# Optimization experiments

Hardware: AMD Instinct MI355X
Metric: run time of the kernel (lower is better)

Reference implementation:

```python
import jax, jax.numpy as jnp
import numpy as np

EPS = 1e-8

def _l2norm(x):
    return x / (jnp.linalg.norm(x, axis=-1, keepdims=True) + EPS)

def setup_inputs() -> dict:
    key = jax.random.key(0)
    k1, k2, k3, k4, k5, k6 = jax.random.split(key, 6)
    NQ, NB, NF = 16384, 128, 64
    HD = 2 * NF
    Q = jax.random.normal(k1, (NQ, HD), dtype=jnp.float32)
    reference_angles = jax.random.uniform(k2, (NF,), dtype=jnp.float32) * 2.0 * np.pi
    probes = jax.random.normal(k3, (NB, HD), dtype=jnp.float32)
    # params: perturb around the torch inits (log(e-1), zeros, zeros) for a non-degenerate test
    init_val = float(np.log(np.e - 1.0))
    q_weights_raw = init_val + 0.1 * jax.random.normal(k4, (NB, NF), dtype=jnp.float32)
    q_magnitude_weights = 0.1 * jax.random.normal(k5, (NB, NF), dtype=jnp.float32)
    q_bias = 0.1 * jax.random.normal(k6, (NB,), dtype=jnp.float32)
    return {"Q": Q, "reference_angles": reference_angles, "probes": probes,
            "q_weights_raw": q_weights_raw, "q_magnitude_weights": q_magnitude_weights,
            "q_bias": q_bias}

def reference(Q, reference_angles, probes, q_weights_raw, q_magnitude_weights, q_bias):
    NF = reference_angles.shape[0]
    # --- shared probe layer: L2 normalize then RoPE-rotate (front/back real/imag layout)
    pn = _l2norm(probes)                      # (B, 2F)
    pr, pi = pn[:, :NF], pn[:, NF:]
    c, s = jnp.cos(reference_angles), jnp.sin(reference_angles)
    P_real = pr * c - pi * s                  # (B, F)
    P_imag = pr * s + pi * c
    # --- distance-based scorer
    Qn = _l2norm(Q)                           # (Nq, 2F)
    Q_real, Q_imag = Qn[:, :NF], Qn[:, NF:]
    err_r = P_real[None, :, :] - Q_real[:, None, :]   # (Nq, B, F)
    err_i = P_imag[None, :, :] - Q_imag[:, None, :]
    distance = jnp.sqrt(err_r ** 2 + err_i ** 2 + EPS)
    eff_w = -jax.nn.softplus(q_weights_raw)           # (B, F), negative weights
    distance_term = jnp.einsum('qbf,bf->qb', distance, eff_w)
    Q_mag = jnp.sqrt(Q_real ** 2 + Q_imag ** 2 + EPS)  # (Nq, F)
    magnitude_term = Q_mag @ q_magnitude_weights.T     # (Nq, B)
    return distance_term + magnitude_term + q_bias
```

## Files before the change

### kernel.cpp

```cpp
#include <hip/hip_runtime.h>

#define NQ 16384
#define NB 128
#define NF 64
#define HD 128
#define EPSF 1e-8f
#define BTILE 8
#define NBT (NB / BTILE)
#define NFP (NF / 2)

typedef float f32x2 __attribute__((ext_vector_type(2)));
typedef float f32x4 __attribute__((ext_vector_type(4)));

struct FP2Row {
    f32x2 x2[BTILE];
    f32x2 y2[BTILE];
    f32x2 z2[BTILE];
    f32x2 w2[BTILE];
    f32x2 m2[BTILE];
};

__global__ __launch_bounds__(256) void prep_kernel(
    const float* __restrict__ Q,
    const float* __restrict__ probes,
    const float* __restrict__ angles,
    const float* __restrict__ qw,
    const float* __restrict__ mw,
    f32x4* __restrict__ qA,
    FP2Row* __restrict__ tab) {
    __shared__ f32x4 sA[8][NFP + 1];
    if (blockIdx.x < 2048) {
        const int qi = threadIdx.x >> 5;
        const int sl = threadIdx.x & 31;
        const int q  = blockIdx.x * 8 + qi;
        const float2* Q2 = (const float2*)Q;
        float2 a = Q2[q * 64 + sl];
        float2 c = Q2[q * 64 + 32 + sl];
        float ss = a.x * a.x + a.y * a.y + c.x * c.x + c.y * c.y;
        #pragma unroll
        for (int m = 1; m < 32; m <<= 1) ss += __shfl_xor(ss, m);
        float inv = 1.0f / (sqrtf(ss) + EPSF);
        f32x4 Av;
        Av.x = a.x * inv; Av.y = a.y * inv;
        Av.z = c.x * inv; Av.w = c.y * inv;
        sA[qi][sl] = Av;
        __syncthreads();
        const int sl2 = threadIdx.x >> 3;
        const int qi2 = threadIdx.x & 7;
        const int qb  = blockIdx.x * 8;
        qA[sl2 * NQ + qb + qi2] = sA[qi2][sl2];
    } else {
        const int b = (blockIdx.x - 2048) * 4 + (threadIdx.x >> 6);
        const int f = threadIdx.x & 63;
        float p0 = probes[b * HD + f];
        float p1 = probes[b * HD + 64 + f];
        float ss = p0 * p0 + p1 * p1;
        #pragma unroll
        for (int m = 1; m < 64; m <<= 1) ss += __shfl_xor(ss, m);
        float inv = 1.0f / (sqrtf(ss) + EPSF);
        float pr = p0 * inv, pi = p1 * inv;
        float ang = angles[f];
        float cc = cosf(ang), sn = sinf(ang);
        float Pr = pr * cc - pi * sn;
        float Pi = pr * sn + pi * cc;
        float x = qw[b * NF + f];
        float sp = (x > 0.0f) ? (x + log1pf(expf(-x))) : log1pf(expf(x));
        FP2Row* r = &tab[(b >> 3) * NFP + (f >> 1)];
        const int h  = f & 1;
        const int bb = b & 7;
        ((float*)&r->x2[bb])[h] = -2.0f * Pr;
        ((float*)&r->y2[bb])[h] = -2.0f * Pi;
        ((float*)&r->z2[bb])[h] = Pr * Pr + Pi * Pi + EPSF;
        ((float*)&r->w2[bb])[h] = -sp;
        ((float*)&r->m2[bb])[h] = mw[b * NF + f];
    }
}

__global__ __launch_bounds__(256, 4) void main_kernel(
    const FP2Row* __restrict__ tab,
    const f32x4* __restrict__ qA,
    const float* __restrict__ bias,
    float* __restrict__ out) {
    const int p    = blockIdx.x;
    const int xcd  = p & 7;
    const int j    = p >> 3;
    const int qblk = xcd * 8 + (j >> 4);
    const int bt   = j & 15;
    const int q    = qblk * 256 + threadIdx.x;

    const FP2Row* __restrict__ tr = tab + bt * NFP;

    f32x2 acc[BTILE];
    #pragma unroll
    for (int i = 0; i < BTILE; ++i) acc[i] = 0.0f;

    f32x4 A = qA[q];
    for (int fp = 0; fp < NFP; ++fp) {
        const int fpn = (fp < NFP - 1) ? fp + 1 : fp;
        f32x4 An = qA[fpn * NQ + q];
        f32x2 qr2 = __builtin_shufflevector(A, A, 0, 1);
        f32x2 qi2 = __builtin_shufflevector(A, A, 2, 3);
        f32x2 qz2 = qr2 * qr2;
        qz2 = __builtin_elementwise_fma(qi2, qi2, qz2);
        f32x2 qm2;
        qm2.x = __builtin_amdgcn_sqrtf(qz2.x + EPSF);
        qm2.y = __builtin_amdgcn_sqrtf(qz2.y + EPSF);
        const FP2Row* r = tr + fp;
        #pragma unroll
        for (int bb = 0; bb < BTILE; ++bb) {
            f32x2 t = r->z2[bb] + qz2;
            t = __builtin_elementwise_fma(r->y2[bb], qi2, t);
            t = __builtin_elementwise_fma(r->x2[bb], qr2, t);
            f32x2 d;
            d.x = __builtin_amdgcn_sqrtf(__builtin_fabsf(t.x));
            d.y = __builtin_amdgcn_sqrtf(__builtin_fabsf(t.y));
            acc[bb] = __builtin_elementwise_fma(r->w2[bb], d, acc[bb]);
            acc[bb] = __builtin_elementwise_fma(r->m2[bb], qm2, acc[bb]);
        }
        A = An;
    }

    float o[BTILE];
    #pragma unroll
    for (int bb = 0; bb < BTILE; ++bb)
        o[bb] = acc[bb].x + acc[bb].y + bias[bt * BTILE + bb];
    float* op = out + (size_t)q * NB + bt * BTILE;
    *(float4*)op       = make_float4(o[0], o[1], o[2], o[3]);
    *(float4*)(op + 4) = make_float4(o[4], o[5], o[6], o[7]);
}

extern "C" void kernel_launch(void* const* d_in, const int* in_sizes, int n_in,
                              void* d_out, int out_size, void* d_ws, size_t ws_size,
                              hipStream_t stream) {
    const float* Q      = (const float*)d_in[0];
    const float* angles = (const float*)d_in[1];
    const float* probes = (const float*)d_in[2];
    const float* qw     = (const float*)d_in[3];
    const float* mw     = (const float*)d_in[4];
    const float* bias   = (const float*)d_in[5];
    float* out = (float*)d_out;

    char* ws = (char*)d_ws;
    FP2Row* tab = (FP2Row*)ws;
    f32x4*  qA  = (f32x4*)(ws + NBT * NFP * sizeof(FP2Row));

    prep_kernel<<<2048 + NB / 4, 256, 0, stream>>>(Q, probes, angles, qw, mw, qA, tab);
    main_kernel<<<(NQ / 256) * NBT, 256, 0, stream>>>(tab, qA, bias, out);
}
```

Before: 99.21 us.

## Share normalized Q tile in LDS across four probe tiles per block

The main kernel moves from 256-thread blocks, each covering one probe tile, to 1024-thread blocks where four probe tiles share one 256-query chunk. The query vectors are staged into shared memory in two halves, so each query row is read from global memory once per block rather than once per probe tile. This cuts global and L2 traffic for qA. In exchange it adds block-wide barriers, uses 64KB of LDS per block, and reduces the grid to 256 large blocks, which may lower occupancy and limit latency hiding.

```diff
diff --git a/kernel.cpp b/kernel.cpp
--- a/kernel.cpp
+++ b/kernel.cpp
@@ -8,6 +8,7 @@
 #define BTILE 8
 #define NBT (NB / BTILE)
 #define NFP (NF / 2)
+#define FPH (NFP / 2)
 
 typedef float f32x2 __attribute__((ext_vector_type(2)));
 typedef float f32x4 __attribute__((ext_vector_type(4)));
@@ -76,17 +77,21 @@
     }
 }
 
-__global__ __launch_bounds__(256, 4) void main_kernel(
+__global__ __launch_bounds__(1024, 4) void main_kernel(
     const FP2Row* __restrict__ tab,
     const f32x4* __restrict__ qA,
     const float* __restrict__ bias,
     float* __restrict__ out) {
-    const int p    = blockIdx.x;
-    const int xcd  = p & 7;
-    const int j    = p >> 3;
-    const int qblk = xcd * 8 + (j >> 4);
-    const int bt   = j & 15;
-    const int q    = qblk * 256 + threadIdx.x;
+    __shared__ f32x4 sA[FPH * 256];
+    const int p     = blockIdx.x;
+    const int xcd   = p & 7;
+    const int j     = p >> 3;
+    const int chunk = xcd * 8 + (j >> 2);
+    const int btq   = j & 3;
+    const int tq    = threadIdx.x & 255;
+    const int bt    = btq * 4 + (threadIdx.x >> 8);
+    const int qbase = chunk * 256;
+    const int q     = qbase + tq;
 
     const FP2Row* __restrict__ tr = tab + bt * NFP;
 
@@ -94,30 +99,42 @@
     #pragma unroll
     for (int i = 0; i < BTILE; ++i) acc[i] = 0.0f;
 
-    f32x4 A = qA[q];
-    for (int fp = 0; fp < NFP; ++fp) {
-        const int fpn = (fp < NFP - 1) ? fp + 1 : fp;
-        f32x4 An = qA[fpn * NQ + q];
-        f32x2 qr2 = __builtin_shufflevector(A, A, 0, 1);
-        f32x2 qi2 = __builtin_shufflevector(A, A, 2, 3);
-        f32x2 qz2 = qr2 * qr2;
-        qz2 = __builtin_elementwise_fma(qi2, qi2, qz2);
-        f32x2 qm2;
-        qm2.x = __builtin_amdgcn_sqrtf(qz2.x + EPSF);
-        qm2.y = __builtin_amdgcn_sqrtf(qz2.y + EPSF);
-        const FP2Row* r = tr + fp;
+    #pragma unroll
+    for (int half = 0; half < 2; ++half) {
+        if (half) __syncthreads();
         #pragma unroll
-        for (int bb = 0; bb < BTILE; ++bb) {
-            f32x2 t = r->z2[bb] + qz2;
-            t = __builtin_elementwise_fma(r->y2[bb], qi2, t);
-            t = __builtin_elementwise_fma(r->x2[bb], qr2, t);
-            f32x2 d;
-            d.x = __builtin_amdgcn_sqrtf(__builtin_fabsf(t.x));
-            d.y = __builtin_amdgcn_sqrtf(__builtin_fabsf(t.y));
-            acc[bb] = __builtin_elementwise_fma(r->w2[bb], d, acc[bb]);
-            acc[bb] = __builtin_elementwise_fma(r->m2[bb], qm2, acc[bb]);
+        for (int k = 0; k < 4; ++k) {
+            int idx = k * 1024 + threadIdx.x;
+            sA[idx] = qA[(half * FPH + (idx >> 8)) * NQ + qbase + (idx & 255)];
         }
-        A = An;
+        __syncthreads();
+
+        f32x4 A = sA[tq];
+        #pragma unroll 4
+        for (int fpl = 0; fpl < FPH; ++fpl) {
+            const int fpln = (fpl < FPH - 1) ? fpl + 1 : fpl;
+            f32x4 An = sA[fpln * 256 + tq];
+            f32x2 qr2 = __builtin_shufflevector(A, A, 0, 1);
+            f32x2 qi2 = __builtin_shufflevector(A, A, 2, 3);
+            f32x2 qz2 = qr2 * qr2;
+            qz2 = __builtin_elementwise_fma(qi2, qi2, qz2);
+            f32x2 qm2;
+            qm2.x = __builtin_amdgcn_sqrtf(qz2.x + EPSF);
+            qm2.y = __builtin_amdgcn_sqrtf(qz2.y + EPSF);
+            const FP2Row* r = tr + half * FPH + fpl;
+            #pragma unroll
+            for (int bb = 0; bb < BTILE; ++bb) {
+                f32x2 t = r->z2[bb] + qz2;
+                t = __builtin_elementwise_fma(r->y2[bb], qi2, t);
+                t = __builtin_elementwise_fma(r->x2[bb], qr2, t);
+                f32x2 d;
+                d.x = __builtin_amdgcn_sqrtf(__builtin_fabsf(t.x));
+                d.y = __builtin_amdgcn_sqrtf(__builtin_fabsf(t.y));
+                acc[bb] = __builtin_elementwise_fma(r->w2[bb], d, acc[bb]);
+                acc[bb] = __builtin_elementwise_fma(r->m2[bb], qm2, acc[bb]);
+            }
+            A = An;
+        }
     }
 
     float o[BTILE];
@@ -145,5 +162,5 @@
     f32x4*  qA  = (f32x4*)(ws + NBT * NFP * sizeof(FP2Row));
 
     prep_kernel<<<2048 + NB / 4, 256, 0, stream>>>(Q, probes, angles, qw, mw, qA, tab);
-    main_kernel<<<(NQ / 256) * NBT, 256, 0, stream>>>(tab, qA, bias, out);
+    main_kernel<<<256, 1024, 0, stream>>>(tab, qA, bias, out);
 }
```

Result: slower. 152.6 us (+53.9%).
